# Performance work log

Measured on AMD Instinct MI355X. Metric: run time of the kernel, lower is better.

## Reference

```python
import jax, jax.numpy as jnp
import numpy as np

VOCAB = 11322
EMB = 300
HID = 512
B, K, T = 64, 100, 20
NUM_QT = 84
NUM_ANS = 30000


def _lstm_layer(x, lens, w_ih, w_hh, b_ih, b_hh):
    """x: [N, T, in], lens: [N]. PyTorch gate order i,f,g,o.
    Returns (outputs [N, T, H], final hidden at t == len-1 [N, H])."""
    N = x.shape[0]
    H = w_hh.shape[1]
    x_t = jnp.swapaxes(x, 0, 1)  # [T, N, in]
    ts = jnp.arange(x.shape[1])

    def step(carry, inp):
        h, c = carry
        xt, t = inp
        gates = xt @ w_ih.T + h @ w_hh.T + (b_ih + b_hh)  # [N, 4H]
        i, f, g, o = jnp.split(gates, 4, axis=-1)
        c_new = jax.nn.sigmoid(f) * c + jax.nn.sigmoid(i) * jnp.tanh(g)
        h_new = jax.nn.sigmoid(o) * jnp.tanh(c_new)
        mask = (t < lens)[:, None]  # freeze state past each seq's length
        h = jnp.where(mask, h_new, h)
        c = jnp.where(mask, c_new, c)
        return (h, c), h

    init = (jnp.zeros((N, H), x.dtype), jnp.zeros((N, H), x.dtype))
    (h_fin, _), ys = jax.lax.scan(step, init, (x_t, ts))
    return jnp.swapaxes(ys, 0, 1), h_fin


def setup_inputs() -> dict:
    key = jax.random.key(0)
    ks = jax.random.split(key, 16)
    s = 1.0 / np.sqrt(HID)
    W_embed = jax.random.normal(ks[0], (VOCAB, EMB), jnp.float32) * 0.02
    W_embed = W_embed.at[0].set(0.0)  # padding_idx=0
    inp = {
        'encoder_output': jax.random.normal(ks[1], (B, HID), jnp.float32),
        'opt': jax.random.randint(ks[2], (B, K, T), 0, VOCAB),
        'opt_len': jax.random.randint(ks[3], (B, K), 1, T + 1),
        'qt_idx': jax.random.randint(ks[4], (B,), 0, NUM_QT),
        'opt_idx': jax.random.randint(ks[5], (B, K), 0, NUM_ANS),
        'W_embed': W_embed,
        'w_ih0': jax.random.uniform(ks[6], (4 * HID, EMB), jnp.float32, -s, s),
        'w_hh0': jax.random.uniform(ks[7], (4 * HID, HID), jnp.float32, -s, s),
        'b_ih0': jax.random.uniform(ks[8], (4 * HID,), jnp.float32, -s, s),
        'b_hh0': jax.random.uniform(ks[9], (4 * HID,), jnp.float32, -s, s),
        'w_ih1': jax.random.uniform(ks[10], (4 * HID, HID), jnp.float32, -s, s),
        'w_hh1': jax.random.uniform(ks[11], (4 * HID, HID), jnp.float32, -s, s),
        'b_ih1': jax.random.uniform(ks[12], (4 * HID,), jnp.float32, -s, s),
        'b_hh1': jax.random.uniform(ks[13], (4 * HID,), jnp.float32, -s, s),
        'relevance': jax.random.uniform(ks[14], (NUM_QT, NUM_ANS)) < 0.02,
    }
    return inp


def reference(encoder_output, opt, opt_len, qt_idx, opt_idx, W_embed,
              w_ih0, w_hh0, b_ih0, b_hh0, w_ih1, w_hh1, b_ih1, b_hh1,
              relevance):
    bsz, num_opt, max_len = opt.shape
    options = opt.reshape(-1, max_len)            # [B*K, T]
    lens = opt_len.reshape(-1)                    # [B*K]
    emb = W_embed[options] * (options != 0)[..., None].astype(W_embed.dtype)
    ys1, _ = _lstm_layer(emb, lens, w_ih0, w_hh0, b_ih0, b_hh0)
    _, h2 = _lstm_layer(ys1, lens, w_ih1, w_hh1, b_ih1, b_hh1)
    options_feat = h2.reshape(bsz, num_opt, HID)
    scores = jnp.einsum('bkh,bh->bk', options_feat, encoder_output)
    # vectorized replacement of the per-sample dict-lookup loop
    qt_score = relevance[qt_idx[:, None], opt_idx].astype(scores.dtype)
    return scores, qt_score
```

## Files before the change

kernel.cpp:

```cpp
#include <hip/hip_runtime.h>

#define NSEQ 6400
#define TMAX 20
#define EMB 300
#define EMBP 320
#define HID 512
#define KL0 832
#define KL1 1024
#define NQT 84
#define NANS 30000
#define RELN (NQT * NANS)

typedef __bf16 bf16x8 __attribute__((ext_vector_type(8)));
typedef float f32x4 __attribute__((ext_vector_type(4)));
typedef unsigned short u16;

__device__ __forceinline__ u16 f2bf(float f) {
  union { float f; unsigned int i; } v; v.f = f;
  unsigned int r = v.i + 0x7fffu + ((v.i >> 16) & 1u);
  return (u16)(r >> 16);
}

__global__ __launch_bounds__(320) void embed_kernel(
    const int* __restrict__ opt, const float* __restrict__ Wemb, u16* __restrict__ embT) {
  int n = blockIdx.x;
  int e = threadIdx.x;
#pragma unroll 4
  for (int t = 0; t < TMAX; ++t) {
    int tok = opt[n * TMAX + t];
    float v = 0.f;
    if (e < EMB && tok != 0) v = Wemb[(size_t)tok * EMB + e];
    embT[((size_t)t * NSEQ + n) * EMBP + e] = f2bf(v);
  }
}

__global__ void prep_w0(const float* __restrict__ wih, const float* __restrict__ whh,
                        u16* __restrict__ W) {
  for (int idx = blockIdx.x * blockDim.x + threadIdx.x; idx < 2048 * KL0;
       idx += gridDim.x * blockDim.x) {
    int o = idx / KL0, c = idx % KL0;
    float v;
    if (c < EMB) v = wih[o * EMB + c];
    else if (c < EMBP) v = 0.f;
    else v = whh[o * HID + (c - EMBP)];
    W[idx] = f2bf(v);
  }
}
__global__ void prep_w1(const float* __restrict__ wih, const float* __restrict__ whh,
                        u16* __restrict__ W) {
  for (int idx = blockIdx.x * blockDim.x + threadIdx.x; idx < 2048 * KL1;
       idx += gridDim.x * blockDim.x) {
    int o = idx / KL1, c = idx % KL1;
    float v = (c < HID) ? wih[o * HID + c] : whh[o * HID + (c - HID)];
    W[idx] = f2bf(v);
  }
}
__global__ void prep_bias(const float* __restrict__ a, const float* __restrict__ b,
                          float* __restrict__ o) {
  int i = blockIdx.x * blockDim.x + threadIdx.x;
  if (i < 2048) o[i] = a[i] + b[i];
}

__global__ __launch_bounds__(512, 2) void lstm_step(
    const u16* __restrict__ segA0, int strideA0, int K0,
    const u16* __restrict__ segA1,
    const u16* __restrict__ Wcat, int Ktot, int nkt,
    const float* __restrict__ biasc,
    u16* __restrict__ h_new, float* __restrict__ c_state,
    const float* __restrict__ hf_old, float* __restrict__ hf_new,
    const int* __restrict__ lens, int t) {
  __shared__ __align__(16) u16 Abuf[2][256 * 64];
  __shared__ __align__(16) u16 Bbuf[2][256 * 64];
  const int tid = threadIdx.x;
  const int wave = tid >> 6, lane = tid & 63;
  const int l15 = lane & 15, l4 = lane >> 4;
  const int mw = wave >> 1, nw = wave & 1;

  const int orig = blockIdx.x;
  const int wgid = (orig & 7) * 25 + (orig >> 3);
  const int rowBlk = (wgid >> 3) * 256;
  const int hblk = (wgid & 7) * 64;

  const int srow = tid >> 3;
  const int sslot = (tid & 7) ^ (srow & 7);

  auto stageA = [&](int sel, int hb, int kt) {
    const int kbase = kt * 64;
    const bool s1 = kbase >= K0;
#pragma unroll
    for (int i = 0; i < 2; ++i) {
      int lrow = hb * 128 + i * 64 + srow;
      int gr = rowBlk + lrow;
      const u16* src = s1 ? (segA1 + (size_t)gr * HID + (kbase - K0) + sslot * 8)
                          : (segA0 + (size_t)gr * strideA0 + kbase + sslot * 8);
      __builtin_amdgcn_global_load_lds(
          (const __attribute__((address_space(1))) void*)src,
          (__attribute__((address_space(3))) void*)(&Abuf[sel][lrow * 64 + (tid & 7) * 8]),
          16, 0, 0);
    }
  };
  auto stageB = [&](int sel, int hb, int kt) {
    const int kbase = kt * 64;
#pragma unroll
    for (int i = 0; i < 2; ++i) {
      int lrow = hb * 128 + i * 64 + srow;
      int g = hb * 2 + i;
      const u16* src = Wcat + (size_t)(g * HID + hblk + srow) * Ktot + kbase + sslot * 8;
      __builtin_amdgcn_global_load_lds(
          (const __attribute__((address_space(1))) void*)src,
          (__attribute__((address_space(3))) void*)(&Bbuf[sel][lrow * 64 + (tid & 7) * 8]),
          16, 0, 0);
    }
  };

  f32x4 acc[4][8] = {};
  bf16x8 a[2][2], bLo[4][2], bHi[4][2];

  auto rdA = [&](int sel, int mhalf) {
#pragma unroll
    for (int mf = 0; mf < 2; ++mf)
#pragma unroll
      for (int ks = 0; ks < 2; ++ks) {
        int row = mw * 64 + mhalf * 32 + mf * 16 + l15;
        int q = (ks * 4 + l4) ^ (row & 7);
        a[mf][ks] = *(const bf16x8*)&Abuf[sel][row * 64 + q * 8];
      }
  };
  auto rdB = [&](int sel, int nhalf, bf16x8 b[4][2]) {
#pragma unroll
    for (int f = 0; f < 4; ++f)
#pragma unroll
      for (int ks = 0; ks < 2; ++ks) {
        int nf = nhalf * 4 + f;
        int row = (nf >> 1) * 64 + nw * 32 + (nf & 1) * 16 + l15;
        int q = (ks * 4 + l4) ^ (row & 7);
        b[f][ks] = *(const bf16x8*)&Bbuf[sel][row * 64 + q * 8];
      }
  };
  auto mma = [&](bf16x8 b[4][2], int mhalf, int nhalf) {
    __builtin_amdgcn_s_setprio(1);
#pragma unroll
    for (int mf = 0; mf < 2; ++mf)
#pragma unroll
      for (int f = 0; f < 4; ++f)
#pragma unroll
        for (int ks = 0; ks < 2; ++ks)
          acc[mhalf * 2 + mf][nhalf * 4 + f] = __builtin_amdgcn_mfma_f32_16x16x32_bf16(
              a[mf][ks], b[f][ks], acc[mhalf * 2 + mf][nhalf * 4 + f], 0, 0, 0);
    __builtin_amdgcn_s_setprio(0);
  };

  stageA(0, 0, 0); stageA(0, 1, 0); stageB(0, 0, 0); stageB(0, 1, 0);
  asm volatile("s_waitcnt vmcnt(0)" ::: "memory");
  __builtin_amdgcn_s_barrier();

  for (int kt = 0; kt < nkt; ++kt) {
    const int cur = kt & 1, nxt = cur ^ 1;
    const bool pf = (kt + 1 < nkt);
    rdA(cur, 0); rdB(cur, 0, bLo);
    if (pf) stageA(nxt, 0, kt + 1);
    __builtin_amdgcn_s_barrier();
    mma(bLo, 0, 0);
    __builtin_amdgcn_s_barrier();
    rdB(cur, 1, bHi);
    if (pf) stageA(nxt, 1, kt + 1);
    __builtin_amdgcn_s_barrier();
    mma(bHi, 0, 1);
    __builtin_amdgcn_s_barrier();
    rdA(cur, 1);
    if (pf) stageB(nxt, 0, kt + 1);
    __builtin_amdgcn_s_barrier();
    mma(bHi, 1, 1);
    __builtin_amdgcn_s_barrier();
    if (pf) stageB(nxt, 1, kt + 1);
    mma(bLo, 1, 0);
    if (pf) asm volatile("s_waitcnt vmcnt(0)" ::: "memory");
    __builtin_amdgcn_s_barrier();
  }

#pragma unroll
  for (int hs = 0; hs < 2; ++hs) {
    const int uu = hblk + nw * 32 + hs * 16 + l15;
    const float bi = biasc[uu], bff = biasc[512 + uu];
    const float bgg = biasc[1024 + uu], bo = biasc[1536 + uu];
#pragma unroll
    for (int m = 0; m < 4; ++m) {
      const int rbase = rowBlk + mw * 64 + m * 16 + l4 * 4;
      const size_t cmi = (size_t)uu * NSEQ + rbase;
      f32x4 co4 = *(const f32x4*)(c_state + cmi);
      int4 ln4 = *(const int4*)(lens + rbase);
      f32x4 ho4;
      if (hf_new) ho4 = *(const f32x4*)(hf_old + cmi);
      f32x4 cn4, hn4;
      u16 hstore[4];
#pragma unroll
      for (int jj = 0; jj < 4; ++jj) {
        float ip = acc[m][hs][jj] + bi;
        float fp = acc[m][2 + hs][jj] + bff;
        float gp = acc[m][4 + hs][jj] + bgg;
        float op = acc[m][6 + hs][jj] + bo;
        float co = co4[jj];
        float si = 1.f / (1.f + __expf(-ip));
        float sf = 1.f / (1.f + __expf(-fp));
        float so = 1.f / (1.f + __expf(-op));
        float tg = tanhf(gp);
        float cn = sf * co + si * tg;
        float hn = so * tanhf(cn);
        int len = (jj == 0) ? ln4.x : (jj == 1) ? ln4.y : (jj == 2) ? ln4.z : ln4.w;
        bool act = t < len;
        cn4[jj] = act ? cn : co;
        hstore[jj] = act ? f2bf(hn) : segA1[(size_t)(rbase + jj) * HID + uu];
        if (hf_new) hn4[jj] = act ? hn : ho4[jj];
      }
      *(f32x4*)(c_state + cmi) = cn4;
      if (hf_new) *(f32x4*)(hf_new + cmi) = hn4;
#pragma unroll
      for (int jj = 0; jj < 4; ++jj)
        h_new[(size_t)(rbase + jj) * HID + uu] = hstore[jj];
    }
  }
}

__global__ __launch_bounds__(256) void scores_kernel(
    const float* __restrict__ h2cm, const float* __restrict__ enc, float* __restrict__ out) {
  int n = (blockIdx.x >> 1) * 256 + threadIdx.x;
  int uh = (blockIdx.x & 1) * 256;
  const float* ep = enc + (n / 100) * HID + uh;
  float s = 0.f;
#pragma unroll 8
  for (int u = 0; u < 256; ++u) s += h2cm[(size_t)(uh + u) * NSEQ + n] * ep[u];
  atomicAdd(&out[n], s);
}

__global__ void detect_kernel(const unsigned char* __restrict__ rel, int* __restrict__ flags) {
  int a = 0, bb = 0, z = 0;
  for (int i = blockIdx.x * blockDim.x + threadIdx.x; i < RELN; i += gridDim.x * blockDim.x) {
    if (rel[i]) {
      if (i & 3) a = 1; else z = 1;
      if (i & 4) bb = 1;
    }
  }
  if (a) atomicOr(&flags[0], 1);
  if (bb) atomicOr(&flags[1], 1);
  if (z) atomicOr(&flags[2], 1);
}

__global__ void qt_kernel(const void* __restrict__ rel, const int* __restrict__ qt_idx,
                          const int* __restrict__ opt_idx, const int* __restrict__ flags,
                          float* __restrict__ out) {
  int n = blockIdx.x * blockDim.x + threadIdx.x;
  if (n >= NSEQ) return;
  long long idx = (long long)qt_idx[n / 100] * NANS + opt_idx[n];
  int fa = flags[0], fb = flags[1], fz = flags[2];
  bool hit;
  if (fa && fz)       hit = ((const unsigned char*)rel)[idx] != 0;
  else if (fa)        hit = ((const float*)rel)[idx] != 0.f;
  else if (fb)        hit = ((const int*)rel)[idx] != 0;
  else                hit = ((const long long*)rel)[idx] != 0;
  out[NSEQ + n] = hit ? 1.f : 0.f;
}

extern "C" void kernel_launch(void* const* d_in, const int* in_sizes, int n_in,
                              void* d_out, int out_size, void* d_ws, size_t ws_size,
                              hipStream_t stream) {
  (void)in_sizes; (void)n_in; (void)out_size; (void)ws_size;
  const float* enc    = (const float*)d_in[0];
  const int*   opt    = (const int*)d_in[1];
  const int*   optlen = (const int*)d_in[2];
  const int*   qtidx  = (const int*)d_in[3];
  const int*   optidx = (const int*)d_in[4];
  const float* Wemb   = (const float*)d_in[5];
  const float* wih0   = (const float*)d_in[6];
  const float* whh0   = (const float*)d_in[7];
  const float* bih0   = (const float*)d_in[8];
  const float* bhh0   = (const float*)d_in[9];
  const float* wih1   = (const float*)d_in[10];
  const float* whh1   = (const float*)d_in[11];
  const float* bih1   = (const float*)d_in[12];
  const float* bhh1   = (const float*)d_in[13];
  const void*  rel    = d_in[14];
  float* out = (float*)d_out;

  char* ws = (char*)d_ws;
  size_t off = 0;
  auto alloc = [&](size_t bytes) -> void* {
    void* p = (void*)(ws + off);
    off += (bytes + 255) & ~(size_t)255;
    return p;
  };
  u16* embT   = (u16*)alloc((size_t)TMAX * NSEQ * EMBP * 2);
  u16* W0     = (u16*)alloc((size_t)2048 * KL0 * 2);
  u16* W1     = (u16*)alloc((size_t)2048 * KL1 * 2);
  float* bc0  = (float*)alloc(2048 * 4);
  float* bc1  = (float*)alloc(2048 * 4);
  u16* h0b[2] = { (u16*)alloc((size_t)NSEQ * HID * 2), (u16*)alloc((size_t)NSEQ * HID * 2) };
  u16* h1b[2] = { (u16*)alloc((size_t)NSEQ * HID * 2), (u16*)alloc((size_t)NSEQ * HID * 2) };
  float* c0   = (float*)alloc((size_t)NSEQ * HID * 4);
  float* c1   = (float*)alloc((size_t)NSEQ * HID * 4);
  float* hf[2] = { (float*)alloc((size_t)NSEQ * HID * 4), (float*)alloc((size_t)NSEQ * HID * 4) };
  int* flags  = (int*)alloc(16);

  hipMemsetAsync(h0b[0], 0, (size_t)NSEQ * HID * 2, stream);
  hipMemsetAsync(h1b[0], 0, (size_t)NSEQ * HID * 2, stream);
  hipMemsetAsync(c0, 0, (size_t)NSEQ * HID * 4, stream);
  hipMemsetAsync(c1, 0, (size_t)NSEQ * HID * 4, stream);
  hipMemsetAsync(hf[0], 0, (size_t)NSEQ * HID * 4, stream);
  hipMemsetAsync(flags, 0, 16, stream);
  hipMemsetAsync(out, 0, (size_t)NSEQ * 4, stream);

  embed_kernel<<<NSEQ, EMBP, 0, stream>>>(opt, Wemb, embT);
  prep_w0<<<512, 256, 0, stream>>>(wih0, whh0, W0);
  prep_w1<<<512, 256, 0, stream>>>(wih1, whh1, W1);
  prep_bias<<<8, 256, 0, stream>>>(bih0, bhh0, bc0);
  prep_bias<<<8, 256, 0, stream>>>(bih1, bhh1, bc1);
  detect_kernel<<<256, 256, 0, stream>>>((const unsigned char*)rel, flags);

  for (int t = 0; t < TMAX; ++t) {
    int cur = t & 1, nxt = cur ^ 1;
    lstm_step<<<200, 512, 0, stream>>>(
        embT + (size_t)t * NSEQ * EMBP, EMBP, EMBP,
        h0b[cur], W0, KL0, KL0 / 64, bc0,
        h0b[nxt], c0, nullptr, nullptr, optlen, t);
    lstm_step<<<200, 512, 0, stream>>>(
        h0b[nxt], HID, HID,
        h1b[cur], W1, KL1, KL1 / 64, bc1,
        h1b[nxt], c1, hf[cur], hf[nxt], optlen, t);
  }

  scores_kernel<<<50, 256, 0, stream>>>(hf[0], enc, out);
  qt_kernel<<<(NSEQ + 255) / 256, 256, 0, stream>>>(rel, qtidx, optidx, flags, out);
}
```

Baseline: 2.139 ms.

## Sort sequences by length and skip finished row blocks in LSTM steps

Builds a length histogram, scan and scatter to permute sequences in descending length order. Embeddings, LSTM state and final scores then work in this sorted order. Each LSTM step exits early for 256-row blocks whose rows have all finished, since arr[t] counts sequences still active at step t. The final hidden state is now written in place only for active rows, which removes the double-buffered copy. The prefetch staging is also regrouped so the next A and B tiles are issued earlier. The cost is a few small extra kernels and an indirection through the permutation.

```diff
diff --git a/kernel.cpp b/kernel.cpp
--- a/kernel.cpp
+++ b/kernel.cpp
@@ -21,16 +21,41 @@
   return (u16)(r >> 16);
 }
 
+__global__ void hist_kernel(const int* __restrict__ lens, int* __restrict__ hist) {
+  int n = blockIdx.x * blockDim.x + threadIdx.x;
+  if (n < NSEQ) atomicAdd(&hist[lens[n]], 1);
+}
+__global__ void scan_kernel(const int* __restrict__ hist, int* __restrict__ arr) {
+  if (threadIdx.x == 0) {
+    int s = 0;
+    arr[21] = 0;
+    for (int l = 20; l >= 1; --l) { s += hist[l]; arr[l] = s; }
+    arr[0] = NSEQ;
+  }
+}
+__global__ void scatter_kernel(const int* __restrict__ lens, const int* __restrict__ arr,
+                               int* __restrict__ cursor, int* __restrict__ perm,
+                               int* __restrict__ lens_s) {
+  int n = blockIdx.x * blockDim.x + threadIdx.x;
+  if (n >= NSEQ) return;
+  int len = lens[n];
+  int pos = arr[len + 1] + atomicAdd(&cursor[len], 1);
+  perm[pos] = n;
+  lens_s[pos] = len;
+}
+
 __global__ __launch_bounds__(320) void embed_kernel(
-    const int* __restrict__ opt, const float* __restrict__ Wemb, u16* __restrict__ embT) {
-  int n = blockIdx.x;
+    const int* __restrict__ opt, const float* __restrict__ Wemb,
+    const int* __restrict__ perm, u16* __restrict__ embT) {
+  int pos = blockIdx.x;
+  int orig = perm[pos];
   int e = threadIdx.x;
 #pragma unroll 4
   for (int t = 0; t < TMAX; ++t) {
-    int tok = opt[n * TMAX + t];
+    int tok = opt[orig * TMAX + t];
     float v = 0.f;
     if (e < EMB && tok != 0) v = Wemb[(size_t)tok * EMB + e];
-    embT[((size_t)t * NSEQ + n) * EMBP + e] = f2bf(v);
+    embT[((size_t)t * NSEQ + pos) * EMBP + e] = f2bf(v);
   }
 }
 
@@ -67,19 +92,21 @@
     const u16* __restrict__ Wcat, int Ktot, int nkt,
     const float* __restrict__ biasc,
     u16* __restrict__ h_new, float* __restrict__ c_state,
-    const float* __restrict__ hf_old, float* __restrict__ hf_new,
-    const int* __restrict__ lens, int t) {
+    float* __restrict__ hfB,
+    const int* __restrict__ lens, const int* __restrict__ activeArr, int t) {
+  const int activeCnt = activeArr[t];
+  const int orig = blockIdx.x;
+  const int wgid = (orig & 7) * 25 + (orig >> 3);
+  const int rowBlk = (wgid >> 3) * 256;
+  const int hblk = (wgid & 7) * 64;
+  if (rowBlk >= activeCnt) return;
+
   __shared__ __align__(16) u16 Abuf[2][256 * 64];
   __shared__ __align__(16) u16 Bbuf[2][256 * 64];
   const int tid = threadIdx.x;
   const int wave = tid >> 6, lane = tid & 63;
   const int l15 = lane & 15, l4 = lane >> 4;
   const int mw = wave >> 1, nw = wave & 1;
-
-  const int orig = blockIdx.x;
-  const int wgid = (orig & 7) * 25 + (orig >> 3);
-  const int rowBlk = (wgid >> 3) * 256;
-  const int hblk = (wgid & 7) * 64;
 
   const int srow = tid >> 3;
   const int sslot = (tid & 7) ^ (srow & 7);
@@ -158,21 +185,19 @@
     const int cur = kt & 1, nxt = cur ^ 1;
     const bool pf = (kt + 1 < nkt);
     rdA(cur, 0); rdB(cur, 0, bLo);
-    if (pf) stageA(nxt, 0, kt + 1);
+    if (pf) { stageA(nxt, 0, kt + 1); stageA(nxt, 1, kt + 1); }
     __builtin_amdgcn_s_barrier();
     mma(bLo, 0, 0);
     __builtin_amdgcn_s_barrier();
     rdB(cur, 1, bHi);
-    if (pf) stageA(nxt, 1, kt + 1);
+    if (pf) { stageB(nxt, 0, kt + 1); stageB(nxt, 1, kt + 1); }
     __builtin_amdgcn_s_barrier();
     mma(bHi, 0, 1);
     __builtin_amdgcn_s_barrier();
     rdA(cur, 1);
-    if (pf) stageB(nxt, 0, kt + 1);
     __builtin_amdgcn_s_barrier();
     mma(bHi, 1, 1);
     __builtin_amdgcn_s_barrier();
-    if (pf) stageB(nxt, 1, kt + 1);
     mma(bLo, 1, 0);
     if (pf) asm volatile("s_waitcnt vmcnt(0)" ::: "memory");
     __builtin_amdgcn_s_barrier();
@@ -189,9 +214,7 @@
       const size_t cmi = (size_t)uu * NSEQ + rbase;
       f32x4 co4 = *(const f32x4*)(c_state + cmi);
       int4 ln4 = *(const int4*)(lens + rbase);
-      f32x4 ho4;
-      if (hf_new) ho4 = *(const f32x4*)(hf_old + cmi);
-      f32x4 cn4, hn4;
+      f32x4 cn4;
       u16 hstore[4];
 #pragma unroll
       for (int jj = 0; jj < 4; ++jj) {
@@ -210,10 +233,9 @@
         bool act = t < len;
         cn4[jj] = act ? cn : co;
         hstore[jj] = act ? f2bf(hn) : segA1[(size_t)(rbase + jj) * HID + uu];
-        if (hf_new) hn4[jj] = act ? hn : ho4[jj];
+        if (hfB && act) hfB[cmi + jj] = hn;
       }
       *(f32x4*)(c_state + cmi) = cn4;
-      if (hf_new) *(f32x4*)(hf_new + cmi) = hn4;
 #pragma unroll
       for (int jj = 0; jj < 4; ++jj)
         h_new[(size_t)(rbase + jj) * HID + uu] = hstore[jj];
@@ -222,14 +244,16 @@
 }
 
 __global__ __launch_bounds__(256) void scores_kernel(
-    const float* __restrict__ h2cm, const float* __restrict__ enc, float* __restrict__ out) {
-  int n = (blockIdx.x >> 1) * 256 + threadIdx.x;
+    const float* __restrict__ h2cm, const float* __restrict__ enc,
+    const int* __restrict__ perm, float* __restrict__ out) {
+  int pos = (blockIdx.x >> 1) * 256 + threadIdx.x;
   int uh = (blockIdx.x & 1) * 256;
-  const float* ep = enc + (n / 100) * HID + uh;
+  int orig = perm[pos];
+  const float* ep = enc + (orig / 100) * HID + uh;
   float s = 0.f;
 #pragma unroll 8
-  for (int u = 0; u < 256; ++u) s += h2cm[(size_t)(uh + u) * NSEQ + n] * ep[u];
-  atomicAdd(&out[n], s);
+  for (int u = 0; u < 256; ++u) s += h2cm[(size_t)(uh + u) * NSEQ + pos] * ep[u];
+  atomicAdd(&out[orig], s);
 }
 
 __global__ void detect_kernel(const unsigned char* __restrict__ rel, int* __restrict__ flags) {
@@ -297,18 +321,27 @@
   u16* h1b[2] = { (u16*)alloc((size_t)NSEQ * HID * 2), (u16*)alloc((size_t)NSEQ * HID * 2) };
   float* c0   = (float*)alloc((size_t)NSEQ * HID * 4);
   float* c1   = (float*)alloc((size_t)NSEQ * HID * 4);
-  float* hf[2] = { (float*)alloc((size_t)NSEQ * HID * 4), (float*)alloc((size_t)NSEQ * HID * 4) };
+  float* hfB  = (float*)alloc((size_t)NSEQ * HID * 4);
   int* flags  = (int*)alloc(16);
+  int* hist   = (int*)alloc(32 * 4);
+  int* arr    = (int*)alloc(32 * 4);
+  int* cursor = (int*)alloc(32 * 4);
+  int* perm   = (int*)alloc(NSEQ * 4);
+  int* lens_s = (int*)alloc(NSEQ * 4);
 
   hipMemsetAsync(h0b[0], 0, (size_t)NSEQ * HID * 2, stream);
   hipMemsetAsync(h1b[0], 0, (size_t)NSEQ * HID * 2, stream);
   hipMemsetAsync(c0, 0, (size_t)NSEQ * HID * 4, stream);
   hipMemsetAsync(c1, 0, (size_t)NSEQ * HID * 4, stream);
-  hipMemsetAsync(hf[0], 0, (size_t)NSEQ * HID * 4, stream);
   hipMemsetAsync(flags, 0, 16, stream);
+  hipMemsetAsync(hist, 0, 32 * 4, stream);
+  hipMemsetAsync(cursor, 0, 32 * 4, stream);
   hipMemsetAsync(out, 0, (size_t)NSEQ * 4, stream);
 
-  embed_kernel<<<NSEQ, EMBP, 0, stream>>>(opt, Wemb, embT);
+  hist_kernel<<<(NSEQ + 255) / 256, 256, 0, stream>>>(optlen, hist);
+  scan_kernel<<<1, 64, 0, stream>>>(hist, arr);
+  scatter_kernel<<<(NSEQ + 255) / 256, 256, 0, stream>>>(optlen, arr, cursor, perm, lens_s);
+  embed_kernel<<<NSEQ, EMBP, 0, stream>>>(opt, Wemb, perm, embT);
   prep_w0<<<512, 256, 0, stream>>>(wih0, whh0, W0);
   prep_w1<<<512, 256, 0, stream>>>(wih1, whh1, W1);
   prep_bias<<<8, 256, 0, stream>>>(bih0, bhh0, bc0);
@@ -320,13 +353,13 @@
     lstm_step<<<200, 512, 0, stream>>>(
         embT + (size_t)t * NSEQ * EMBP, EMBP, EMBP,
         h0b[cur], W0, KL0, KL0 / 64, bc0,
-        h0b[nxt], c0, nullptr, nullptr, optlen, t);
+        h0b[nxt], c0, nullptr, lens_s, arr, t);
     lstm_step<<<200, 512, 0, stream>>>(
         h0b[nxt], HID, HID,
         h1b[cur], W1, KL1, KL1 / 64, bc1,
-        h1b[nxt], c1, hf[cur], hf[nxt], optlen, t);
-  }
-
-  scores_kernel<<<50, 256, 0, stream>>>(hf[0], enc, out);
+        h1b[nxt], c1, hfB, lens_s, arr, t);
+  }
+
+  scores_kernel<<<50, 256, 0, stream>>>(hfB, enc, perm, out);
   qt_kernel<<<(NSEQ + 255) / 256, 256, 0, stream>>>(rel, qtidx, optidx, flags, out);
 }
```

After: 2.026 ms. 5.3% less time.
